# Kernel tuning notes

Measured on AMD Instinct MI355X. Metric: run time of the kernel, lower is better.

## Reference

```python
import jax, jax.numpy as jnp
import numpy as np

B, S, L, CIN = 8, 32, 128, 1024
C1, C2 = 512, 256            # conv1_channel, conv2_channel
D1, D2 = 512, 128            # deconv1_channel, deconv2_channel
CD, SIM = 300, 128           # concept_dim, similarity_dim
L4 = L // 4


def _conv1d(x, w, b, pad):
    # x: [N, Cin, L], w: [Cout, Cin, k] (PyTorch layout)
    y = jax.lax.conv_general_dilated(x, w, (1,), [(pad, pad)],
                                     dimension_numbers=('NCH', 'OIH', 'NCH'))
    return y + b[None, :, None]


def _maxpool2(x):
    return jax.lax.reduce_window(x, -jnp.inf, jax.lax.max, (1, 1, 2), (1, 1, 2), 'VALID')


def _deconv1d(x, w, b):
    # PyTorch ConvTranspose1d(kernel=4, stride=2, padding=1); w: [Cin, Cout, k]
    w2 = jnp.flip(w, -1).transpose(1, 0, 2)  # -> OIH
    y = jax.lax.conv_general_dilated(x, w2, (1,), [(2, 2)], lhs_dilation=(2,),
                                     dimension_numbers=('NCH', 'OIH', 'NCH'))
    return y + b[None, :, None]


def setup_inputs():
    ks = jax.random.split(jax.random.key(0), 32)
    g = lambda i, shape: jax.random.normal(ks[i], shape, jnp.float32) * 0.02
    return {
        'batch': jax.random.normal(ks[0], (B, S, L, CIN), jnp.float32),
        'concept1': jax.random.normal(ks[1], (B, CD), jnp.float32),
        'concept2': jax.random.normal(ks[2], (B, CD), jnp.float32),
        'seg_len': jax.random.randint(ks[3], (B, S), 1, L + 1),
        'conv1_w': g(4, (C1, CIN, 5)), 'conv1_b': g(5, (C1,)),
        'conv2_w': g(6, (C2, C1, 5)), 'conv2_b': g(7, (C2,)),
        'sa_wq': g(8, (C2, C2)), 'sa_bq': g(9, (C2,)),
        'sa_wk': g(10, (C2, C2)), 'sa_bk': g(11, (C2,)),
        'sa_v': g(12, (C2,)), 'sa_vb': g(13, ()),
        'ca_wq': g(14, (CD, C2)), 'ca_bq': g(15, (C2,)),
        'ca_wk': g(16, (C2, C2)), 'ca_bk': g(17, (C2,)),
        'ca_v': g(18, (C2,)), 'ca_vb': g(19, ()),
        'dc1_w': g(20, (4 * C2, D1, 4)), 'dc1_b': g(21, (D1,)),
        'dc2_w': g(22, (D1, D2, 4)), 'dc2_b': g(23, (D2,)),
        'sim1_w': g(24, (D2, SIM)),
        'sim2_w': g(25, (CD, SIM)),
        'mlp_w': g(26, (SIM,)), 'mlp_b': g(27, ()),
    }


def reference(batch, concept1, concept2, seg_len,
              conv1_w, conv1_b, conv2_w, conv2_b,
              sa_wq, sa_bq, sa_wk, sa_bk, sa_v, sa_vb,
              ca_wq, ca_bq, ca_wk, ca_bk, ca_v, ca_vb,
              dc1_w, dc1_b, dc2_w, dc2_b,
              sim1_w, sim2_w, mlp_w, mlp_b):
    N = B * S
    # conv stack: [N, CIN, L] -> [N, C2, L/4]
    x = batch.reshape(N, L, CIN).transpose(0, 2, 1)
    t = _maxpool2(_conv1d(x, conv1_w, conv1_b, 2))
    t = _maxpool2(_conv1d(t, conv2_w, conv2_b, 2))
    tmp2 = t.transpose(0, 2, 1)                       # [N, L4, C2]

    # vectorized length mask: mask[i,j,k] = k < ceil(seg_len/4)  <=>  seg_len > 4k
    mask = (seg_len[:, :, None] > 4 * jnp.arange(L4)).reshape(N, 1, L4)

    # self additive attention over pooled positions
    qp = tmp2 @ sa_wq + sa_bq                          # [N, L4, H]
    kp = tmp2 @ sa_wk + sa_bk                          # [N, L4, H]
    s = jnp.einsum('nqkh,h->nqk', jnp.tanh(qp[:, :, None, :] + kp[:, None, :, :]), sa_v) + sa_vb
    s = jnp.where(mask, s, -1e9)
    a = jax.nn.softmax(s, axis=-1)                     # [N, L4, L4]
    self_res = jnp.einsum('nqk,nkc->nqc', a, tmp2)     # [N, L4, C2]

    # concept attention (query identical across positions -> compute once)
    ckp = tmp2 @ ca_wk + ca_bk                         # [N, L4, H]

    def concept_attn(c):
        cq = jnp.repeat(c @ ca_wq + ca_bq, S, axis=0)  # [N, H]
        sc = jnp.einsum('nkh,h->nk', jnp.tanh(cq[:, None, :] + ckp), ca_v) + ca_vb
        sc = jnp.where(mask[:, 0, :], sc, -1e9)
        ac = jax.nn.softmax(sc, axis=-1)               # [N, L4]
        r = jnp.einsum('nk,nkc->nc', ac, tmp2)         # [N, C2]
        return jnp.broadcast_to(r[:, None, :], (N, L4, C2))

    c1_res = concept_attn(concept1)
    c2_res = concept_attn(concept2)

    ar = jnp.concatenate([tmp2, self_res, c1_res, c2_res], axis=-1)  # [N, L4, 4*C2]
    r = _deconv1d(ar.transpose(0, 2, 1), dc1_w, dc1_b)               # [N, D1, L/2]
    r = _deconv1d(r, dc2_w, dc2_b).transpose(0, 2, 1)                # [N, L, D2]
    r = r.reshape(B, S * L, D2)

    sim1 = r @ sim1_w                                                # [B, S*L, SIM]

    def score(c):
        cs = (c @ sim2_w)[:, None, :] * sim1
        return jax.nn.sigmoid(cs @ mlp_w + mlp_b).reshape(B, S, L)

    return score(concept1), score(concept2)
```

## Files before the change

### kernel.cpp

```cpp
#include <hip/hip_runtime.h>
#include <cstdint>

typedef __bf16 bf16;
typedef __bf16 bf16x8 __attribute__((ext_vector_type(8)));
typedef float f32x4 __attribute__((ext_vector_type(4)));
typedef __attribute__((address_space(3))) bf16 lds_bf16;

__device__ __forceinline__ void gload_lds16(const void* g, void* l) {
  __builtin_amdgcn_global_load_lds(
      (const __attribute__((address_space(1))) unsigned int*)g,
      (__attribute__((address_space(3))) unsigned int*)l, 16, 0, 0);
}

__device__ __forceinline__ bf16x8 ld_b128(const lds_bf16* p) {
  bf16x8 r;
  asm volatile("ds_read_b128 %0, %1" : "=v"(r) : "v"(p));
  return r;
}

__device__ __forceinline__ float tanh_fast(float x) {
  float ax = fabsf(x);
  float e = __expf(ax + ax);
  float t = 1.0f - 2.0f / (e + 1.0f);
  return x < 0.0f ? -t : t;
}

template<int MODE, int DEPTH>
__global__ __launch_bounds__(256) void gemm_tap(
    const bf16* __restrict__ A, const bf16* __restrict__ Bt,
    const float* __restrict__ bias, bf16* __restrict__ Out,
    const bf16* __restrict__ zp,
    int snA, int logP, int logCI, int shift0, int ntaps, int cbCount,
    int cbCI, int pairs, int Ktot, int COt, int snO,
    const float* __restrict__ uu, const float* __restrict__ mlpb,
    float* __restrict__ outF)
{
  __shared__ __align__(16) bf16 Ab[2 * DEPTH][4096];
  __shared__ __align__(16) bf16 Bb[2 * DEPTH][4096];
  const int tid  = threadIdx.x;
  const int wave = tid >> 6, lane = tid & 63;
  const int wr = wave >> 1, wc = wave & 1;
  const int m0  = blockIdx.x << 7;
  const int co0 = blockIdx.y << 7;
  const int P     = 1 << logP;
  const int Pmask = P - 1;
  const int CI    = 1 << logCI;
  f32x4 acc[4][4] = {};

  const int rowL = tid >> 2;
  const int kg   = tid & 3;
  const int fOff = ((kg ^ ((rowL + (rowL >> 2)) & 3)) << 3);

  const int mA0 = m0 + rowL,      nA0 = mA0 >> logP, pA0v = mA0 & Pmask;
  const int mA1 = m0 + rowL + 64, nA1 = mA1 >> logP, pA1v = mA1 & Pmask;
  const bf16* baseA0 = A + nA0 * snA + fOff;
  const bf16* baseA1 = A + nA1 * snA + fOff;
  const bf16* baseB0 = Bt + (co0 + rowL) * Ktot + fOff;
  const bf16* baseB1 = Bt + (co0 + rowL + 64) * Ktot + fOff;
  const bf16* zsrc = zp + fOff;

  const int frow  = lane & 15;
  const int rdOff = (((lane >> 4) ^ ((frow + (frow >> 2)) & 3)) << 3);

  for (int cb = 0; cb < cbCount; ++cb) {
    for (int tap = 0; tap < ntaps; ++tap) {
      const int sh = tap + shift0;
      const int rA0 = pA0v + sh, rA1 = pA1v + sh;
      const bool v0 = (unsigned)rA0 < (unsigned)P;
      const bool v1 = (unsigned)rA1 < (unsigned)P;
      const bf16* pa0 = v0 ? (baseA0 + rA0 * CI + cb * cbCI) : zsrc;
      const bf16* pa1 = v1 ? (baseA1 + rA1 * CI + cb * cbCI) : zsrc;
      const bf16* pb0 = baseB0 + (cb * ntaps + tap) * cbCI;
      const bf16* pb1 = baseB1 + (cb * ntaps + tap) * cbCI;

      for (int kc = 0; kc < pairs; kc += DEPTH) {
#pragma unroll
        for (int h = 0; h < 2 * DEPTH; ++h) {
          gload_lds16(pa0 + 32 * h, &Ab[h][wave * 512]);
          gload_lds16(pa1 + 32 * h, &Ab[h][2048 + wave * 512]);
          gload_lds16(pb0 + 32 * h, &Bb[h][wave * 512]);
          gload_lds16(pb1 + 32 * h, &Bb[h][2048 + wave * 512]);
        }
        if (v0) pa0 += 64 * DEPTH;
        if (v1) pa1 += 64 * DEPTH;
        pb0 += 64 * DEPTH; pb1 += 64 * DEPTH;
        __syncthreads();
#pragma unroll
        for (int h = 0; h < 2 * DEPTH; ++h) {
          bf16x8 af[4], bg[4];
#pragma unroll
          for (int i = 0; i < 4; ++i) {
            af[i] = *(const bf16x8*)&Ab[h][((wr << 6) + (i << 4) + frow) * 32 + rdOff];
            bg[i] = *(const bf16x8*)&Bb[h][((wc << 6) + (i << 4) + frow) * 32 + rdOff];
          }
#pragma unroll
          for (int i = 0; i < 4; ++i)
#pragma unroll
            for (int j = 0; j < 4; ++j)
              acc[i][j] = __builtin_amdgcn_mfma_f32_16x16x32_bf16(af[i], bg[j], acc[i][j], 0, 0, 0);
        }
        __syncthreads();
      }
    }
  }

  const int colL = lane & 15;
  const int rq   = (lane >> 4) << 2;

  if (MODE == 2) {
    float* scr0 = (float*)&Ab[0][0];
    float* scr1 = (float*)&Bb[0][0];
    const int n = m0 >> logP;
    const int b = n >> 5;
    const float* u0 = uu + b * 128;
    const float* u1 = uu + 1024 + b * 128;
#pragma unroll
    for (int i = 0; i < 4; ++i) {
#pragma unroll
      for (int r = 0; r < 4; ++r) {
        int rowLcl = (wr << 6) + (i << 4) + rq + r;
        float p0 = 0.0f, p1 = 0.0f;
#pragma unroll
        for (int j = 0; j < 4; ++j) {
          int gco = (wc << 6) + (j << 4) + colL;
          float v = acc[i][j][r];
          p0 += v * u0[gco];
          p1 += v * u1[gco];
        }
        scr0[rowLcl * 32 + (wc << 4) + colL] = p0;
        scr1[rowLcl * 32 + (wc << 4) + colL] = p1;
      }
    }
    __syncthreads();
    {
      int rowLcl = tid >> 1, c = tid & 1;
      const float* s = c ? scr1 : scr0;
      float sum = 0.0f;
#pragma unroll
      for (int k = 0; k < 32; ++k) sum += s[rowLcl * 32 + k];
      float val = 1.0f / (1.0f + __expf(-(sum + mlpb[0])));
      outF[(c ? 32768 : 0) + m0 + rowLcl] = val;
    }
    return;
  }

#pragma unroll
  for (int i = 0; i < 4; ++i) {
    int m = m0 + (wr << 6) + (i << 4) + rq;
    int n = m >> logP, p = m & Pmask;
#pragma unroll
    for (int j = 0; j < 4; ++j) {
      int gco = co0 + (wc << 6) + (j << 4) + colL;
      float bv = bias[gco];
      if (MODE == 1) {
        float v0 = fmaxf(acc[i][j][0], acc[i][j][1]) + bv;
        float v1 = fmaxf(acc[i][j][2], acc[i][j][3]) + bv;
        bf16* o = Out + n * snO + (p >> 1) * COt + gco;
        o[0]   = (bf16)v0;
        o[COt] = (bf16)v1;
      } else {
#pragma unroll
        for (int r = 0; r < 4; ++r)
          Out[n * snO + (p + r) * COt + gco] = (bf16)(acc[i][j][r] + bv);
      }
    }
  }
}

template<int MH, int KS, typename F>
__device__ __forceinline__ void phase8(
    const bf16 (&Ab)[2][2][8192], const bf16 (&Bb)[2][2][8192],
    f32x4 (&acc)[8][4], int buf, int wr, int wc, int frow, int rdOff,
    F&& stage)
{
  bf16x8 af[4], bg[4];
#pragma unroll
  for (int ii = 0; ii < 4; ++ii)
    af[ii] = ld_b128((const lds_bf16*)&Ab[buf][KS][((wr << 7) + (MH << 6) + (ii << 4) + frow) * 32 + rdOff]);
#pragma unroll
  for (int j = 0; j < 4; ++j)
    bg[j] = ld_b128((const lds_bf16*)&Bb[buf][KS][((wc << 6) + (j << 4) + frow) * 32 + rdOff]);
  stage();
  __builtin_amdgcn_s_barrier();
  asm volatile("s_waitcnt lgkmcnt(0)" ::: "memory");
  __builtin_amdgcn_sched_barrier(0);
  __builtin_amdgcn_s_setprio(1);
#pragma unroll
  for (int ii = 0; ii < 4; ++ii)
#pragma unroll
    for (int j = 0; j < 4; ++j)
      acc[(MH << 2) + ii][j] =
          __builtin_amdgcn_mfma_f32_16x16x32_bf16(af[ii], bg[j], acc[(MH << 2) + ii][j], 0, 0, 0);
  __builtin_amdgcn_s_setprio(0);
}

template<int LOGP, int LOGCI, int SH0, int NTAPS, int CBCNT, int CBCI>
__global__ __launch_bounds__(512, 2) void gemm8_pool(
    const bf16* __restrict__ A, const bf16* __restrict__ Bt,
    const float* __restrict__ bias, bf16* __restrict__ Out,
    const bf16* __restrict__ zp, int snA, int Ktot, int COt, int snO)
{
  __shared__ __align__(16) bf16 Ab[2][2][8192];
  __shared__ __align__(16) bf16 Bb[2][2][8192];
  constexpr int P = 1 << LOGP, CI = 1 << LOGCI;
  constexpr int KPC = CBCI / 64;
  constexpr int NT = CBCNT * NTAPS * KPC;

  const int tid = threadIdx.x;
  const int wave = tid >> 6, lane = tid & 63;
  const int wr = wave >> 2, wc = wave & 3;
  const int m0 = blockIdx.x << 8, co0 = blockIdx.y << 8;
  const int n0 = m0 >> LOGP;

  f32x4 acc[8][4] = {};

  const int rowP = tid >> 2;
  const int kOff = (((tid & 3) ^ ((rowP + (rowP >> 2)) & 3)) << 3);
  const bf16* baseA = A + n0 * snA + kOff;
  const bf16* baseB = Bt + (co0 + rowP) * Ktot + kOff;
  const bf16* zsrc = zp + kOff;
  const int ldsW = wave << 9;

  const int frow = lane & 15;
  const int rdOff = (((lane >> 4) ^ ((frow + (frow >> 2)) & 3)) << 3);

  auto stageA = [&](int u, int kh, int bfs) {
    int cb = u / (NTAPS * KPC);
    int rem = u - cb * (NTAPS * KPC);
    int tap = rem / KPC;
    int kc = rem - tap * KPC;
    int rA = rowP + tap + SH0;
    bool v = (unsigned)rA < (unsigned)P;
    const bf16* p0 = v ? baseA + rA * CI + cb * CBCI + kc * 64 + kh * 32 : zsrc;
    const bf16* p1 = v ? p0 + snA : zsrc;
    gload_lds16(p0, &Ab[bfs][kh][ldsW]);
    gload_lds16(p1, &Ab[bfs][kh][ldsW + 4096]);
  };
  auto stageB = [&](int u, int kh, int bfs) {
    const bf16* p0 = baseB + u * 64 + kh * 32;
    gload_lds16(p0, &Bb[bfs][kh][ldsW]);
    gload_lds16(p0 + 128 * Ktot, &Bb[bfs][kh][ldsW + 4096]);
  };

  stageA(0, 0, 0); stageB(0, 0, 0);
  stageA(0, 1, 0); stageB(0, 1, 0);
  stageA(1, 0, 1); stageB(1, 0, 1);
  asm volatile("s_waitcnt vmcnt(4)" ::: "memory");
  __builtin_amdgcn_s_barrier();

#pragma unroll 1
  for (int t = 0; t < NT; ++t) {
    const int buf = t & 1;
    phase8<0, 0>(Ab, Bb, acc, buf, wr, wc, frow, rdOff,
                 [&] { if (t + 1 < NT) stageA(t + 1, 1, buf ^ 1); });
    __builtin_amdgcn_s_barrier();
    phase8<1, 0>(Ab, Bb, acc, buf, wr, wc, frow, rdOff,
                 [&] { if (t + 1 < NT) stageB(t + 1, 1, buf ^ 1); });
    __builtin_amdgcn_s_barrier();
    phase8<0, 1>(Ab, Bb, acc, buf, wr, wc, frow, rdOff,
                 [&] { if (t + 2 < NT) stageA(t + 2, 0, buf); });
    __builtin_amdgcn_s_barrier();
    phase8<1, 1>(Ab, Bb, acc, buf, wr, wc, frow, rdOff,
                 [&] { if (t + 2 < NT) stageB(t + 2, 0, buf); });
    if (t < NT - 2) { asm volatile("s_waitcnt vmcnt(4)" ::: "memory"); }
    else            { asm volatile("s_waitcnt vmcnt(0)" ::: "memory"); }
    __builtin_amdgcn_s_barrier();
  }

  const int colL = lane & 15, rq = (lane >> 4) << 2;
#pragma unroll
  for (int i = 0; i < 8; ++i) {
    int m = m0 + (wr << 7) + (i << 4) + rq;
    int n = m >> LOGP, p = m & (P - 1);
    bf16* orow = Out + n * snO + (p >> 1) * COt;
#pragma unroll
    for (int j = 0; j < 4; ++j) {
      int gco = co0 + (wc << 6) + (j << 4) + colL;
      float bv = bias[gco];
      orow[gco]       = (bf16)(fmaxf(acc[i][j][0], acc[i][j][1]) + bv);
      orow[COt + gco] = (bf16)(fmaxf(acc[i][j][2], acc[i][j][3]) + bv);
    }
  }
}

__global__ __launch_bounds__(256) void prep_all(
    const float* __restrict__ conv1_w, const float* __restrict__ conv2_w,
    const float* __restrict__ sa_wq, const float* __restrict__ sa_wk,
    const float* __restrict__ ca_wk, const float* __restrict__ dc1_w,
    const float* __restrict__ dc2_w, const float* __restrict__ sim1_w,
    const float* __restrict__ c1b, const float* __restrict__ c2b,
    const float* __restrict__ sabq, const float* __restrict__ sabk,
    const float* __restrict__ cabk, const float* __restrict__ d1b,
    const float* __restrict__ d2b,
    const float* __restrict__ c1, const float* __restrict__ c2,
    const float* __restrict__ ca_wq, const float* __restrict__ ca_bq,
    const float* __restrict__ sim2_w, const float* __restrict__ mlp_w,
    const float* __restrict__ batch, bf16* __restrict__ bb16,
    bf16* __restrict__ Bt1, bf16* __restrict__ Bt2, bf16* __restrict__ Bqkc,
    bf16* __restrict__ Btd1, bf16* __restrict__ Btd2, bf16* __restrict__ Bts1,
    float* __restrict__ bias, float* __restrict__ cq, float* __restrict__ uu)
{
  const int blk = blockIdx.x;
  if (blk >= 27492) {
    int idx = ((blk - 27492) * 256 + threadIdx.x) * 8;
    float4 a = *(const float4*)&batch[idx];
    float4 b = *(const float4*)&batch[idx + 4];
    bf16x8 v;
    v[0] = (bf16)a.x; v[1] = (bf16)a.y; v[2] = (bf16)a.z; v[3] = (bf16)a.w;
    v[4] = (bf16)b.x; v[5] = (bf16)b.y; v[6] = (bf16)b.z; v[7] = (bf16)b.w;
    *(bf16x8*)&bb16[idx] = v;
    return;
  }
  if (blk < 27468) {
    int idx = blk * 256 + threadIdx.x;
    if (idx < 3072) {
      if (idx < 2944) {
        float v;
        if (idx < 512)       v = c1b[idx];
        else if (idx < 768)  v = c2b[idx - 512];
        else if (idx < 1024) v = sabq[idx - 768];
        else if (idx < 1280) v = sabk[idx - 1024];
        else if (idx < 1536) v = cabk[idx - 1280];
        else if (idx < 2560) v = d1b[(idx - 1536) & 511];
        else if (idx < 2816) v = d2b[(idx - 2560) & 127];
        else                 v = 0.0f;
        bias[idx] = v;
      }
    } else if (idx < 2624512) {
      int i = idx - 3072;
      int co = i / 5120, r = i - co * 5120;
      int cb = r / 1280, r2 = r - cb * 1280;
      int tap = r2 >> 8, cl = r2 & 255;
      Bt1[i] = (bf16)conv1_w[co * 5120 + (cb * 256 + cl) * 5 + tap];
    } else if (idx < 3279872) {
      int i = idx - 2624512;
      int co = i / 2560, r = i - co * 2560;
      int cb = r / 1280, r2 = r - cb * 1280;
      int tap = r2 >> 8, cl = r2 & 255;
      Bt2[i] = (bf16)conv2_w[co * 2560 + (cb * 256 + cl) * 5 + tap];
    } else if (idx < 3476480) {
      int i = idx - 3279872;
      int co = i >> 8, ci = i & 255;
      float v;
      if (co < 256)      v = sa_wq[ci * 256 + co];
      else if (co < 512) v = sa_wk[ci * 256 + (co - 256)];
      else               v = ca_wk[ci * 256 + (co - 512)];
      Bqkc[i] = (bf16)v;
    } else if (idx < 6622208) {
      int i = idx - 3476480;
      int co = i / 3072, r = i - co * 3072;
      int cb = r / 768, r2 = r - cb * 768;
      int tap = r2 >> 8, cl = r2 & 255;
      int ci = cb * 256 + cl;
      int par = co >> 9, c = co & 511;
      int ki = -1;
      if (par == 0) { if (tap == 1) ki = 1; else if (tap == 0) ki = 3; }
      else          { if (tap == 2) ki = 0; else if (tap == 1) ki = 2; }
      Btd1[i] = (ki >= 0) ? (bf16)dc1_w[ci * 2048 + c * 4 + ki] : (bf16)0.0f;
    } else if (idx < 7015424) {
      int i = idx - 6622208;
      int co = i / 1536, r = i - co * 1536;
      int cb = r / 768, r2 = r - cb * 768;
      int tap = r2 >> 8, cl = r2 & 255;
      int ci = cb * 256 + cl;
      int par = co >> 7, c = co & 127;
      int ki = -1;
      if (par == 0) { if (tap == 1) ki = 1; else if (tap == 0) ki = 3; }
      else          { if (tap == 2) ki = 0; else if (tap == 1) ki = 2; }
      Btd2[i] = (ki >= 0) ? (bf16)dc2_w[ci * 512 + c * 4 + ki] : (bf16)0.0f;
    } else {
      int i = idx - 7015424;
      int co = i >> 7, ci = i & 127;
      Bts1[i] = (bf16)sim1_w[ci * 128 + co];
    }
  } else {
    int sub = blk - 27468;
    if (sub < 16) {
      int o = sub * 256 + threadIdx.x;
      int c = o >> 11, b = (o >> 8) & 7, h = o & 255;
      const float* cc = (c ? c2 : c1) + b * 300;
      float acc = ca_bq[h];
      for (int j = 0; j < 300; ++j)
        acc += cc[j] * ca_wq[j * 256 + h];
      cq[o] = acc;
    } else {
      int o = (sub - 16) * 256 + threadIdx.x;
      int c = o >> 10, b = (o >> 7) & 7, m = o & 127;
      const float* cc = (c ? c2 : c1) + b * 300;
      float acc = 0.0f;
      for (int j = 0; j < 300; ++j)
        acc += cc[j] * sim2_w[j * 128 + m];
      uu[o] = acc * mlp_w[m];
    }
  }
}

__global__ __launch_bounds__(256) void kattn(
    const bf16* __restrict__ tmp2, const bf16* __restrict__ qkc,
    const float* __restrict__ sa_v, const float* __restrict__ sa_vb,
    const float* __restrict__ ca_v, const float* __restrict__ ca_vb,
    const float* __restrict__ cq, const int* __restrict__ seg,
    bf16* __restrict__ ar)
{
  const int n = blockIdx.x, tid = threadIdx.x;
  __shared__ __align__(16) bf16 t2[32 * 264];
  __shared__ __align__(16) bf16 bufA[32 * 264];
  __shared__ __align__(16) bf16 bufB[32 * 264];
  __shared__ float sv_s[256], cv_s[256];
  __shared__ float sbc[66];
  __shared__ float sbs[32 * 33];
  const int sl = seg[n];

#pragma unroll
  for (int rr = 0; rr < 4; ++rr) {
    int q = tid + (rr << 8);
    int k = q >> 5, c8 = (q & 31) << 3;
    *(uint4*)&t2[k * 264 + c8]   = *(const uint4*)&tmp2[n * 8192 + k * 256 + c8];
    *(uint4*)&bufA[k * 264 + c8] = *(const uint4*)&qkc[n * 24576 + k * 768 + 512 + c8];
  }
  sv_s[tid] = sa_v[tid];
  cv_s[tid] = ca_v[tid];
  __syncthreads();

  if (tid < 64) {
    int c = tid >> 5, k = tid & 31;
    const float* cqr = cq + (c * 8 + (n >> 5)) * 256;
    float acc = 0.0f;
    for (int h = 0; h < 256; ++h)
      acc += tanh_fast(cqr[h] + (float)bufA[k * 264 + h]) * cv_s[h];
    float sc = acc + ca_vb[0];
    sbc[c * 33 + k] = (sl > (k << 2)) ? sc : -1e9f;
  }
  __syncthreads();

#pragma unroll
  for (int rr = 0; rr < 4; ++rr) {
    int q = tid + (rr << 8);
    int k = q >> 5, c8 = (q & 31) << 3;
    *(uint4*)&bufB[k * 264 + c8] = *(const uint4*)&qkc[n * 24576 + k * 768 + c8];
    *(uint4*)&bufA[k * 264 + c8] = *(const uint4*)&qkc[n * 24576 + k * 768 + 256 + c8];
  }
  if (tid < 2) {
    float* row = &sbc[tid * 33];
    float mx = -1e30f;
    for (int k = 0; k < 32; ++k) mx = fmaxf(mx, row[k]);
    float sum = 0.0f;
    for (int k = 0; k < 32; ++k) { float e = __expf(row[k] - mx); row[k] = e; sum += e; }
    float inv = 1.0f / sum;
    for (int k = 0; k < 32; ++k) row[k] *= inv;
  }
  __syncthreads();

  {
    int col = tid;
    float rr0 = 0.0f, rr1 = 0.0f;
    for (int k = 0; k < 32; ++k) {
      float tv = (float)t2[k * 264 + col];
      rr0 += sbc[k] * tv;
      rr1 += sbc[33 + k] * tv;
    }
    bf16 b0 = (bf16)rr0, b1 = (bf16)rr1;
    bf16* arn = ar + n * 32768;
    for (int q = 0; q < 32; ++q) {
      arn[q * 1024 + col]       = t2[q * 264 + col];
      arn[q * 1024 + 512 + col] = b0;
      arn[q * 1024 + 768 + col] = b1;
    }
  }
  {
    float svb = sa_vb[0];
#pragma unroll
    for (int rr = 0; rr < 4; ++rr) {
      int id = tid + (rr << 8);
      int q = id >> 5, k = id & 31;
      float acc = 0.0f;
      for (int h = 0; h < 256; ++h)
        acc += tanh_fast((float)bufB[q * 264 + h] + (float)bufA[k * 264 + h]) * sv_s[h];
      float sc = acc + svb;
      sbs[q * 33 + k] = (sl > (k << 2)) ? sc : -1e9f;
    }
  }
  __syncthreads();

  if (tid < 32) {
    float* row = &sbs[tid * 33];
    float mx = -1e30f;
    for (int k = 0; k < 32; ++k) mx = fmaxf(mx, row[k]);
    float sum = 0.0f;
    for (int k = 0; k < 32; ++k) { float e = __expf(row[k] - mx); row[k] = e; sum += e; }
    float inv = 1.0f / sum;
    for (int k = 0; k < 32; ++k) row[k] *= inv;
  }
  __syncthreads();

  {
    int col = tid;
    bf16* arn = ar + n * 32768;
    for (int q = 0; q < 32; ++q) {
      float acc = 0.0f;
      for (int k = 0; k < 32; ++k)
        acc += sbs[q * 33 + k] * (float)t2[k * 264 + col];
      arn[q * 1024 + 256 + col] = (bf16)acc;
    }
  }
}

extern "C" void kernel_launch(void* const* d_in, const int* in_sizes, int n_in,
                              void* d_out, int out_size, void* d_ws, size_t ws_size,
                              hipStream_t stream) {
  const float* batch    = (const float*)d_in[0];
  const float* concept1 = (const float*)d_in[1];
  const float* concept2 = (const float*)d_in[2];
  const int*   seg      = (const int*)d_in[3];
  const float* conv1_w  = (const float*)d_in[4];
  const float* conv1_b  = (const float*)d_in[5];
  const float* conv2_w  = (const float*)d_in[6];
  const float* conv2_b  = (const float*)d_in[7];
  const float* sa_wq    = (const float*)d_in[8];
  const float* sa_bq    = (const float*)d_in[9];
  const float* sa_wk    = (const float*)d_in[10];
  const float* sa_bk    = (const float*)d_in[11];
  const float* sa_v     = (const float*)d_in[12];
  const float* sa_vb    = (const float*)d_in[13];
  const float* ca_wq    = (const float*)d_in[14];
  const float* ca_bq    = (const float*)d_in[15];
  const float* ca_wk    = (const float*)d_in[16];
  const float* ca_bk    = (const float*)d_in[17];
  const float* ca_v     = (const float*)d_in[18];
  const float* ca_vb    = (const float*)d_in[19];
  const float* dc1_w    = (const float*)d_in[20];
  const float* dc1_b    = (const float*)d_in[21];
  const float* dc2_w    = (const float*)d_in[22];
  const float* dc2_b    = (const float*)d_in[23];
  const float* sim1_w   = (const float*)d_in[24];
  const float* sim2_w   = (const float*)d_in[25];
  const float* mlp_w    = (const float*)d_in[26];
  const float* mlp_b    = (const float*)d_in[27];

  char* ws = (char*)d_ws;
  bf16* bb16  = (bf16*)(ws + 0);
  bf16* qkcb  = (bf16*)(ws + 0);
  bf16* arb   = (bf16*)(ws + 12582912);
  bf16* d1    = (bf16*)(ws + 29360128);
  bf16* rbuf  = (bf16*)(ws + 46137344);
  bf16* t1    = (bf16*)(ws + 67108864);
  bf16* tmp2b = (bf16*)(ws + 83886080);
  bf16* Bt1   = (bf16*)(ws + 88080384);
  bf16* Bt2   = (bf16*)(ws + 93323264);
  bf16* Bqkc  = (bf16*)(ws + 94633984);
  bf16* Btd1  = (bf16*)(ws + 95027200);
  bf16* Btd2  = (bf16*)(ws + 101318656);
  bf16* Bts1  = (bf16*)(ws + 102105088);
  float* biasall = (float*)(ws + 102137856);
  float* cqb  = (float*)(ws + 102149632);
  float* uub  = (float*)(ws + 102166016);
  const bf16* zp = (const bf16*)(biasall + 2816);
  float* outp = (float*)d_out;

  prep_all<<<43876, 256, 0, stream>>>(
      conv1_w, conv2_w, sa_wq, sa_wk, ca_wk, dc1_w, dc2_w, sim1_w,
      conv1_b, conv2_b, sa_bq, sa_bk, ca_bk, dc1_b, dc2_b,
      concept1, concept2, ca_wq, ca_bq, sim2_w, mlp_w,
      batch, bb16,
      Bt1, Bt2, Bqkc, Btd1, Btd2, Bts1, biasall, cqb, uub);

  gemm8_pool<7, 10, -2, 5, 4, 256><<<dim3(128, 2), 512, 0, stream>>>(
      bb16, Bt1, biasall + 0, t1, zp, 131072, 5120, 512, 32768);

  gemm_tap<1, 2><<<dim3(128, 2), 256, 0, stream>>>(
      t1, Bt2, biasall + 512, tmp2b, zp, 32768, 6, 9, -2, 5, 2, 256, 4, 2560, 256, 8192,
      nullptr, nullptr, nullptr);

  gemm_tap<0, 2><<<dim3(64, 6), 256, 0, stream>>>(
      tmp2b, Bqkc, biasall + 768, qkcb, zp, 8192, 5, 8, 0, 1, 1, 256, 4, 256, 768, 24576,
      nullptr, nullptr, nullptr);

  kattn<<<256, 256, 0, stream>>>(tmp2b, qkcb, sa_v, sa_vb, ca_v, ca_vb, cqb, seg, arb);

  gemm_tap<0, 2><<<dim3(64, 8), 256, 0, stream>>>(
      arb, Btd1, biasall + 1536, d1, zp, 32768, 5, 10, -1, 3, 4, 256, 4, 3072, 1024, 32768,
      nullptr, nullptr, nullptr);

  gemm_tap<0, 2><<<dim3(128, 2), 256, 0, stream>>>(
      d1, Btd2, biasall + 2560, rbuf, zp, 32768, 6, 9, -1, 3, 2, 256, 4, 1536, 256, 16384,
      nullptr, nullptr, nullptr);

  gemm_tap<2, 2><<<dim3(256, 1), 256, 0, stream>>>(
      rbuf, Bts1, biasall + 2816, nullptr, zp, 16384, 7, 7, 0, 1, 1, 128, 2, 128, 128, 16384,
      uub, mlp_b, outp);
}
```

Before: 671.9 us.

## Restructure conv GEMM main loop into single-barrier double-buffered tile pipeline

Replaces the four-phase loop, which had a barrier per phase and staggered half-tile prefetches, with one prefetch of the whole next K tile per iteration and a single __syncthreads. LDS fragment reads are software-pipelined against the MFMA groups using partial lgkmcnt waits. Tile indices are now advanced incrementally instead of recomputed with divisions. This cuts the number of barriers and the index arithmetic, at the cost of a shallower prefetch distance (one tile ahead rather than staggered halves) and more live registers.

```diff
diff --git a/kernel.cpp b/kernel.cpp
--- a/kernel.cpp
+++ b/kernel.cpp
@@ -167,33 +167,6 @@
   }
 }
 
-template<int MH, int KS, typename F>
-__device__ __forceinline__ void phase8(
-    const bf16 (&Ab)[2][2][8192], const bf16 (&Bb)[2][2][8192],
-    f32x4 (&acc)[8][4], int buf, int wr, int wc, int frow, int rdOff,
-    F&& stage)
-{
-  bf16x8 af[4], bg[4];
-#pragma unroll
-  for (int ii = 0; ii < 4; ++ii)
-    af[ii] = ld_b128((const lds_bf16*)&Ab[buf][KS][((wr << 7) + (MH << 6) + (ii << 4) + frow) * 32 + rdOff]);
-#pragma unroll
-  for (int j = 0; j < 4; ++j)
-    bg[j] = ld_b128((const lds_bf16*)&Bb[buf][KS][((wc << 6) + (j << 4) + frow) * 32 + rdOff]);
-  stage();
-  __builtin_amdgcn_s_barrier();
-  asm volatile("s_waitcnt lgkmcnt(0)" ::: "memory");
-  __builtin_amdgcn_sched_barrier(0);
-  __builtin_amdgcn_s_setprio(1);
-#pragma unroll
-  for (int ii = 0; ii < 4; ++ii)
-#pragma unroll
-    for (int j = 0; j < 4; ++j)
-      acc[(MH << 2) + ii][j] =
-          __builtin_amdgcn_mfma_f32_16x16x32_bf16(af[ii], bg[j], acc[(MH << 2) + ii][j], 0, 0, 0);
-  __builtin_amdgcn_s_setprio(0);
-}
-
 template<int LOGP, int LOGCI, int SH0, int NTAPS, int CBCNT, int CBCI>
 __global__ __launch_bounds__(512, 2) void gemm8_pool(
     const bf16* __restrict__ A, const bf16* __restrict__ Bt,
@@ -217,54 +190,100 @@
   const int rowP = tid >> 2;
   const int kOff = (((tid & 3) ^ ((rowP + (rowP >> 2)) & 3)) << 3);
   const bf16* baseA = A + n0 * snA + kOff;
-  const bf16* baseB = Bt + (co0 + rowP) * Ktot + kOff;
-  const bf16* zsrc = zp + kOff;
+  const bf16* pBs   = Bt + (co0 + rowP) * Ktot + kOff;
+  const bf16* zsrc  = zp + kOff;
   const int ldsW = wave << 9;
+  const int bStride = 128 * Ktot;
 
   const int frow = lane & 15;
   const int rdOff = (((lane >> 4) ^ ((frow + (frow >> 2)) & 3)) << 3);
 
-  auto stageA = [&](int u, int kh, int bfs) {
-    int cb = u / (NTAPS * KPC);
-    int rem = u - cb * (NTAPS * KPC);
-    int tap = rem / KPC;
-    int kc = rem - tap * KPC;
-    int rA = rowP + tap + SH0;
+  int s_kc = 0, s_tap = 0, s_cb = 0;
+
+  auto stageTile = [&](int bfs) {
+    int rA = rowP + s_tap + SH0;
     bool v = (unsigned)rA < (unsigned)P;
-    const bf16* p0 = v ? baseA + rA * CI + cb * CBCI + kc * 64 + kh * 32 : zsrc;
-    const bf16* p1 = v ? p0 + snA : zsrc;
-    gload_lds16(p0, &Ab[bfs][kh][ldsW]);
-    gload_lds16(p1, &Ab[bfs][kh][ldsW + 4096]);
+    const bf16* pA0 = v ? baseA + rA * CI + (s_cb * CBCI + s_kc * 64) : zsrc;
+    const bf16* pA1 = v ? pA0 + snA : zsrc;
+    gload_lds16(pA0,      &Ab[bfs][0][ldsW]);
+    gload_lds16(pA0 + 32, &Ab[bfs][1][ldsW]);
+    gload_lds16(pA1,      &Ab[bfs][0][ldsW + 4096]);
+    gload_lds16(pA1 + 32, &Ab[bfs][1][ldsW + 4096]);
+    gload_lds16(pBs,                &Bb[bfs][0][ldsW]);
+    gload_lds16(pBs + 32,           &Bb[bfs][1][ldsW]);
+    gload_lds16(pBs + bStride,      &Bb[bfs][0][ldsW + 4096]);
+    gload_lds16(pBs + bStride + 32, &Bb[bfs][1][ldsW + 4096]);
+    pBs += 64;
+    if (++s_kc == KPC) { s_kc = 0; if (++s_tap == NTAPS) { s_tap = 0; ++s_cb; } }
   };
-  auto stageB = [&](int u, int kh, int bfs) {
-    const bf16* p0 = baseB + u * 64 + kh * 32;
-    gload_lds16(p0, &Bb[bfs][kh][ldsW]);
-    gload_lds16(p0 + 128 * Ktot, &Bb[bfs][kh][ldsW + 4096]);
+
+  auto ldA = [&](int buf, int ks, int mh, int i) {
+    return ld_b128((const lds_bf16*)
+        &Ab[buf][ks][((wr << 7) + (mh << 6) + (i << 4) + frow) * 32 + rdOff]);
   };
-
-  stageA(0, 0, 0); stageB(0, 0, 0);
-  stageA(0, 1, 0); stageB(0, 1, 0);
-  stageA(1, 0, 1); stageB(1, 0, 1);
-  asm volatile("s_waitcnt vmcnt(4)" ::: "memory");
-  __builtin_amdgcn_s_barrier();
+  auto ldB = [&](int buf, int ks, int j) {
+    return ld_b128((const lds_bf16*)
+        &Bb[buf][ks][((wc << 6) + (j << 4) + frow) * 32 + rdOff]);
+  };
+
+  stageTile(0);
+  __syncthreads();
+
+  bf16x8 a0[4], a1[4], b0[4], b1[4];
 
 #pragma unroll 1
   for (int t = 0; t < NT; ++t) {
     const int buf = t & 1;
-    phase8<0, 0>(Ab, Bb, acc, buf, wr, wc, frow, rdOff,
-                 [&] { if (t + 1 < NT) stageA(t + 1, 1, buf ^ 1); });
-    __builtin_amdgcn_s_barrier();
-    phase8<1, 0>(Ab, Bb, acc, buf, wr, wc, frow, rdOff,
-                 [&] { if (t + 1 < NT) stageB(t + 1, 1, buf ^ 1); });
-    __builtin_amdgcn_s_barrier();
-    phase8<0, 1>(Ab, Bb, acc, buf, wr, wc, frow, rdOff,
-                 [&] { if (t + 2 < NT) stageA(t + 2, 0, buf); });
-    __builtin_amdgcn_s_barrier();
-    phase8<1, 1>(Ab, Bb, acc, buf, wr, wc, frow, rdOff,
-                 [&] { if (t + 2 < NT) stageB(t + 2, 0, buf); });
-    if (t < NT - 2) { asm volatile("s_waitcnt vmcnt(4)" ::: "memory"); }
-    else            { asm volatile("s_waitcnt vmcnt(0)" ::: "memory"); }
-    __builtin_amdgcn_s_barrier();
+#pragma unroll
+    for (int i = 0; i < 4; ++i) a0[i] = ldA(buf, 0, 0, i);
+#pragma unroll
+    for (int j = 0; j < 4; ++j) b0[j] = ldB(buf, 0, j);
+    if (t + 1 < NT) stageTile(buf ^ 1);
+#pragma unroll
+    for (int i = 0; i < 4; ++i) a1[i] = ldA(buf, 0, 1, i);
+    asm volatile("s_waitcnt lgkmcnt(4)" ::: "memory");
+    __builtin_amdgcn_sched_barrier(0);
+    __builtin_amdgcn_s_setprio(1);
+#pragma unroll
+    for (int i = 0; i < 4; ++i)
+#pragma unroll
+      for (int j = 0; j < 4; ++j)
+        acc[i][j] = __builtin_amdgcn_mfma_f32_16x16x32_bf16(a0[i], b0[j], acc[i][j], 0, 0, 0);
+    __builtin_amdgcn_s_setprio(0);
+#pragma unroll
+    for (int i = 0; i < 4; ++i) a0[i] = ldA(buf, 1, 0, i);
+#pragma unroll
+    for (int j = 0; j < 4; ++j) b1[j] = ldB(buf, 1, j);
+    asm volatile("s_waitcnt lgkmcnt(8)" ::: "memory");
+    __builtin_amdgcn_sched_barrier(0);
+    __builtin_amdgcn_s_setprio(1);
+#pragma unroll
+    for (int i = 0; i < 4; ++i)
+#pragma unroll
+      for (int j = 0; j < 4; ++j)
+        acc[4 + i][j] = __builtin_amdgcn_mfma_f32_16x16x32_bf16(a1[i], b0[j], acc[4 + i][j], 0, 0, 0);
+    __builtin_amdgcn_s_setprio(0);
+#pragma unroll
+    for (int i = 0; i < 4; ++i) a1[i] = ldA(buf, 1, 1, i);
+    asm volatile("s_waitcnt lgkmcnt(4)" ::: "memory");
+    __builtin_amdgcn_sched_barrier(0);
+    __builtin_amdgcn_s_setprio(1);
+#pragma unroll
+    for (int i = 0; i < 4; ++i)
+#pragma unroll
+      for (int j = 0; j < 4; ++j)
+        acc[i][j] = __builtin_amdgcn_mfma_f32_16x16x32_bf16(a0[i], b1[j], acc[i][j], 0, 0, 0);
+    __builtin_amdgcn_s_setprio(0);
+    asm volatile("s_waitcnt lgkmcnt(0)" ::: "memory");
+    __builtin_amdgcn_sched_barrier(0);
+    __builtin_amdgcn_s_setprio(1);
+#pragma unroll
+    for (int i = 0; i < 4; ++i)
+#pragma unroll
+      for (int j = 0; j < 4; ++j)
+        acc[4 + i][j] = __builtin_amdgcn_mfma_f32_16x16x32_bf16(a1[i], b1[j], acc[4 + i][j], 0, 0, 0);
+    __builtin_amdgcn_s_setprio(0);
+    __syncthreads();
   }
 
   const int colL = lane & 15, rq = (lane >> 4) << 2;
```

Result: faster. 638.9 us (-4.9%).
